# Performance work log

Measured on AMD Instinct MI355X. Metric: run time of the kernel, lower is better.

## Reference

```python
import jax, jax.numpy as jnp
import numpy as np

# SMPL/STAR kinematic tree: parent of joint i (i = 1..23)
PARENT = np.array([0, 0, 0, 1, 2, 3, 4, 5, 6, 7, 8, 9, 9, 9, 12, 13, 14, 16, 17, 18, 19, 20, 21])
B, V, J, NB = 512, 6890, 24, 10


def _axis_angle_parts(theta):
    # theta: [N,3] axis-angle. Matches STAR: norm of (theta + 1e-8).
    angle = jnp.linalg.norm(theta + 1e-8, axis=1, keepdims=True)  # [N,1]
    normalized = theta / angle
    half = angle * 0.5
    return jnp.cos(half), jnp.sin(half), normalized


def quat_feat(theta):
    c, s, n = _axis_angle_parts(theta)
    return jnp.concatenate([s * n, c - 1.0], axis=1)  # [N,4]


def rodrigues(theta):
    c, s, n = _axis_angle_parts(theta)
    w = c[:, 0]
    xyz = s * n
    x, y, z = xyz[:, 0], xyz[:, 1], xyz[:, 2]
    xx, yy, zz = x * x, y * y, z * z
    wx, wy, wz = w * x, w * y, w * z
    xy, xz, yz = x * y, x * z, y * z
    R = jnp.stack([
        1 - 2 * (yy + zz), 2 * (xy - wz), 2 * (xz + wy),
        2 * (xy + wz), 1 - 2 * (xx + zz), 2 * (yz - wx),
        2 * (xz - wy), 2 * (yz + wx), 1 - 2 * (xx + yy)], axis=-1)
    return R.reshape(-1, 3, 3)


def setup_inputs() -> dict:
    key = jax.random.key(0)
    ks = jax.random.split(key, 8)
    pose = jax.random.normal(ks[0], (B, 72), jnp.float32)
    betas = jax.random.normal(ks[1], (B, NB), jnp.float32)
    trans = jax.random.normal(ks[2], (B, 3), jnp.float32)
    v_template = jax.random.normal(ks[3], (V, 3), jnp.float32)
    shapedirs = jax.random.normal(ks[4], (V * 3, NB), jnp.float32) * 0.01
    posedirs = jax.random.normal(ks[5], (V * 3, 93), jnp.float32) * 0.01
    J_regressor = jax.random.uniform(ks[6], (J, V), jnp.float32)
    J_regressor = J_regressor / jnp.sum(J_regressor, axis=1, keepdims=True)
    weights = jax.random.uniform(ks[7], (V, J), jnp.float32)
    weights = weights / jnp.sum(weights, axis=1, keepdims=True)
    return {"pose": pose, "betas": betas, "trans": trans,
            "v_template": v_template, "shapedirs": shapedirs,
            "posedirs": posedirs, "J_regressor": J_regressor,
            "weights": weights}


def reference(pose, betas, trans, v_template, shapedirs, posedirs, J_regressor, weights):
    b = pose.shape[0]
    # shape blendshapes
    v_shaped = jnp.einsum('dk,bk->bd', shapedirs, betas).reshape(b, V, 3) + v_template[None]
    Jp = jnp.einsum('bik,ji->bjk', v_shaped, J_regressor)
    # pose features: quat feats of joints 1..23 + second beta
    pose_quat = quat_feat(pose.reshape(-1, 3)).reshape(b, -1)   # [b,96]
    pose_feat = jnp.concatenate([pose_quat[:, 4:], betas[:, 1:2]], axis=1)  # [b,93]
    R = rodrigues(pose.reshape(-1, 3)).reshape(b, J, 3, 3)
    # pose blendshapes
    v_posed = v_shaped + jnp.einsum('dk,bk->bd', posedirs, pose_feat).reshape(b, V, 3)
    # relative joint locations
    J_rel = jnp.concatenate([Jp[:, :1], Jp[:, 1:] - Jp[:, PARENT]], axis=1)  # [b,24,3]
    # local transforms [b,24,4,4]
    G_local = jnp.concatenate([R, J_rel[:, :, :, None]], axis=-1)
    pad = jnp.broadcast_to(jnp.array([0., 0., 0., 1.], jnp.float32).reshape(1, 1, 1, 4), (b, J, 1, 4))
    G_local = jnp.concatenate([G_local, pad], axis=2)
    # serial forward kinematics (fixed 24-joint chain)
    Gs = [G_local[:, 0]]
    for i in range(1, J):
        Gs.append(jnp.matmul(Gs[PARENT[i - 1]], G_local[:, i]))
    G = jnp.stack(Gs, axis=1)  # [b,24,4,4]
    posed_joints = G[:, :, :3, 3]
    # remove rest-pose joint transform: translation col -= R_part @ J
    t = jnp.einsum('bjxy,bjy->bjx', G[:, :, :3, :3], Jp)
    G_skin = G.at[:, :, :3, 3].add(-t)
    # skinning: T [b,6890,4,4]
    T = jnp.einsum('vj,bjxy->bvxy', weights, G_skin)
    v_h = jnp.concatenate([v_posed, jnp.ones((b, V, 1), v_posed.dtype)], axis=-1)
    v = jnp.einsum('bvxy,bvy->bvx', T, v_h)[:, :, :3] + trans[:, None, :]
    J_transformed = posed_joints + trans[:, None, :]
    return v, v_posed, v_shaped, J_transformed
```

## Files before the change

### kernel.cpp

```cpp
#include <hip/hip_runtime.h>

constexpr int kB  = 512;
constexpr int kV  = 6890;
constexpr int kJ  = 24;
constexpr int kD  = kV * 3;
constexpr int kNB = 10;
constexpr int kNF = 93;

__global__ __launch_bounds__(256) void kA_js(
    const float* __restrict__ Jreg, const float* __restrict__ shapedirs,
    const float* __restrict__ v_template, float* __restrict__ js,
    float* __restrict__ jt) {
  int jk = blockIdx.x;
  int j = jk / 3, k = jk % 3;
  int tid = threadIdx.x;
  float acc[kNB];
  float accT = 0.f;
#pragma unroll
  for (int nb = 0; nb < kNB; ++nb) acc[nb] = 0.f;
  for (int v = tid; v < kV; v += 256) {
    float w = Jreg[(size_t)j * kV + v];
    const float* srow = shapedirs + (size_t)(v * 3 + k) * kNB;
    accT += w * v_template[v * 3 + k];
#pragma unroll
    for (int nb = 0; nb < kNB; ++nb) acc[nb] += w * srow[nb];
  }
#pragma unroll
  for (int nb = 0; nb < kNB; ++nb)
#pragma unroll
    for (int off = 32; off > 0; off >>= 1)
      acc[nb] += __shfl_down(acc[nb], off, 64);
#pragma unroll
  for (int off = 32; off > 0; off >>= 1) accT += __shfl_down(accT, off, 64);
  __shared__ float red[4][11];
  int wave = tid >> 6, lane = tid & 63;
  if (lane == 0) {
#pragma unroll
    for (int nb = 0; nb < kNB; ++nb) red[wave][nb] = acc[nb];
    red[wave][10] = accT;
  }
  __syncthreads();
  if (tid == 0) {
#pragma unroll
    for (int nb = 0; nb < kNB; ++nb)
      js[jk * kNB + nb] = red[0][nb] + red[1][nb] + red[2][nb] + red[3][nb];
    jt[jk] = red[0][10] + red[1][10] + red[2][10] + red[3][10];
  }
}

__global__ __launch_bounds__(64) void kC_batch(
    const float* __restrict__ pose, const float* __restrict__ betas,
    const float* __restrict__ trans, const float* __restrict__ js,
    const float* __restrict__ jt, float* __restrict__ pfT,
    float* __restrict__ Gskin, float* __restrict__ out_Jt) {
  const int parent[24] = {-1, 0, 0, 0, 1, 2, 3, 4, 5, 6, 7, 8,
                          9, 9, 9, 12, 13, 14, 16, 17, 18, 19, 20, 21};
  const int depth[24] = {0, 1, 1, 1, 2, 2, 2, 3, 3, 3, 4, 4,
                         4, 4, 4, 5, 5, 5, 6, 6, 7, 7, 8, 8};
  int b = blockIdx.x;
  int j = threadIdx.x;
  __shared__ float G[24][12];
  __shared__ float Jp_s[24][3];
  float R[9];
  if (j < 24) {
    float t0 = pose[b * 72 + 3 * j + 0];
    float t1 = pose[b * 72 + 3 * j + 1];
    float t2 = pose[b * 72 + 3 * j + 2];
    float a0 = t0 + 1e-8f, a1 = t1 + 1e-8f, a2 = t2 + 1e-8f;
    float angle = sqrtf(a0 * a0 + a1 * a1 + a2 * a2);
    float inv = 1.0f / angle;
    float h = 0.5f * angle;
    float c = cosf(h), s = sinf(h);
    float x = s * t0 * inv, y = s * t1 * inv, z = s * t2 * inv, w = c;
    if (j >= 1) {
      int f = 4 * (j - 1);
      pfT[(size_t)(f + 0) * kB + b] = x;
      pfT[(size_t)(f + 1) * kB + b] = y;
      pfT[(size_t)(f + 2) * kB + b] = z;
      pfT[(size_t)(f + 3) * kB + b] = c - 1.0f;
    } else {
      pfT[(size_t)92 * kB + b] = betas[b * kNB + 1];
    }
    float xx = x * x, yy = y * y, zz = z * z;
    float wx = w * x, wy = w * y, wz = w * z;
    float xy = x * y, xz = x * z, yz = y * z;
    R[0] = 1.f - 2.f * (yy + zz); R[1] = 2.f * (xy - wz); R[2] = 2.f * (xz + wy);
    R[3] = 2.f * (xy + wz); R[4] = 1.f - 2.f * (xx + zz); R[5] = 2.f * (yz - wx);
    R[6] = 2.f * (xz - wy); R[7] = 2.f * (yz + wx); R[8] = 1.f - 2.f * (xx + yy);
    float bet[kNB];
#pragma unroll
    for (int nb = 0; nb < kNB; ++nb) bet[nb] = betas[b * kNB + nb];
#pragma unroll
    for (int k = 0; k < 3; ++k) {
      float a = jt[j * 3 + k];
      const float* jr = js + (size_t)(j * 3 + k) * kNB;
#pragma unroll
      for (int nb = 0; nb < kNB; ++nb) a += jr[nb] * bet[nb];
      Jp_s[j][k] = a;
    }
  }
  __syncthreads();
  float tl[3];
  if (j < 24) {
    int p = parent[j];
#pragma unroll
    for (int k = 0; k < 3; ++k)
      tl[k] = (p >= 0) ? (Jp_s[j][k] - Jp_s[p][k]) : Jp_s[j][k];
    if (j == 0) {
#pragma unroll
      for (int r = 0; r < 3; ++r) {
        G[0][r * 4 + 0] = R[r * 3 + 0];
        G[0][r * 4 + 1] = R[r * 3 + 1];
        G[0][r * 4 + 2] = R[r * 3 + 2];
        G[0][r * 4 + 3] = tl[r];
      }
    }
  }
  __syncthreads();
  for (int lev = 1; lev <= 8; ++lev) {
    if (j < 24 && depth[j] == lev) {
      int p = parent[j];
      float nG[12];
#pragma unroll
      for (int r = 0; r < 3; ++r) {
        float g0 = G[p][r * 4 + 0], g1 = G[p][r * 4 + 1];
        float g2 = G[p][r * 4 + 2], g3 = G[p][r * 4 + 3];
        nG[r * 4 + 0] = g0 * R[0] + g1 * R[3] + g2 * R[6];
        nG[r * 4 + 1] = g0 * R[1] + g1 * R[4] + g2 * R[7];
        nG[r * 4 + 2] = g0 * R[2] + g1 * R[5] + g2 * R[8];
        nG[r * 4 + 3] = g0 * tl[0] + g1 * tl[1] + g2 * tl[2] + g3;
      }
#pragma unroll
      for (int e = 0; e < 12; ++e) G[j][e] = nG[e];
    }
    __syncthreads();
  }
  if (j < 24) {
    float tr[3];
#pragma unroll
    for (int k = 0; k < 3; ++k) tr[k] = trans[b * 3 + k];
#pragma unroll
    for (int k = 0; k < 3; ++k)
      out_Jt[b * 72 + j * 3 + k] = G[j][k * 4 + 3] + tr[k];
    float jp0 = Jp_s[j][0], jp1 = Jp_s[j][1], jp2 = Jp_s[j][2];
    float* gs = Gskin + b * 288 + j * 12;
#pragma unroll
    for (int r = 0; r < 3; ++r) {
      float t = G[j][r * 4 + 0] * jp0 + G[j][r * 4 + 1] * jp1 + G[j][r * 4 + 2] * jp2;
      gs[r * 4 + 0] = G[j][r * 4 + 0];
      gs[r * 4 + 1] = G[j][r * 4 + 1];
      gs[r * 4 + 2] = G[j][r * 4 + 2];
      gs[r * 4 + 3] = G[j][r * 4 + 3] - t;
    }
  }
}

__global__ __launch_bounds__(256) void k14_fused(
    const float* __restrict__ shapedirs, const float* __restrict__ posedirs,
    const float* __restrict__ v_template, const float* __restrict__ betas,
    const float* __restrict__ pfT, float* __restrict__ out_vshaped,
    float* __restrict__ out_vposed) {
  int tid = threadIdx.x;
  int d = blockIdx.x * 256 + tid;
  bool active = d < kD;
  int dl = active ? d : (kD - 1);
  float sd[kNB], pd[kNF];
#pragma unroll
  for (int k = 0; k < kNB; ++k) sd[k] = shapedirs[(size_t)dl * kNB + k];
#pragma unroll
  for (int f = 0; f < kNF; ++f) pd[f] = posedirs[(size_t)dl * kNF + f];
  float vt = v_template[dl];
  int b0 = blockIdx.y * 32;
#pragma unroll 1
  for (int bc = 0; bc < 4; ++bc) {
    int bb = b0 + bc * 8;
    float as[8], ap[8];
#pragma unroll
    for (int t = 0; t < 8; ++t) {
      float a = vt;
#pragma unroll
      for (int k = 0; k < kNB; ++k) a += sd[k] * betas[(size_t)(bb + t) * kNB + k];
      as[t] = a;
      ap[t] = a;
    }
#pragma unroll
    for (int f = 0; f < kNF; ++f) {
      float pdf = pd[f];
      const float* q = pfT + (size_t)f * kB + bb;
#pragma unroll
      for (int t = 0; t < 8; ++t) ap[t] += pdf * q[t];
    }
    if (active) {
#pragma unroll
      for (int t = 0; t < 8; ++t) {
        size_t idx = (size_t)(bb + t) * kD + d;
        out_vshaped[idx] = as[t];
        out_vposed[idx] = ap[t];
      }
    }
  }
}

__global__ __launch_bounds__(256) void k5_skin(
    const float* __restrict__ weights, const float* __restrict__ Gskin,
    const float* __restrict__ trans, const float* __restrict__ vposed,
    float* __restrict__ out_v) {
  int tid = threadIdx.x;
  int v = blockIdx.x * 256 + tid;
  bool active = v < kV;
  int vl = active ? v : (kV - 1);
  float w[kJ];
#pragma unroll
  for (int j = 0; j < kJ; ++j) w[j] = weights[(size_t)vl * kJ + j];
  int b0 = blockIdx.y * 8;
#pragma unroll 1
  for (int bi = 0; bi < 8; ++bi) {
    int b = b0 + bi;
    const float* Gb = Gskin + (size_t)b * 288;
    float T[12];
#pragma unroll
    for (int e = 0; e < 12; ++e) T[e] = 0.f;
#pragma unroll
    for (int j = 0; j < kJ; ++j) {
      float wj = w[j];
#pragma unroll
      for (int e = 0; e < 12; ++e) T[e] += wj * Gb[j * 12 + e];
    }
    float tr0 = trans[b * 3 + 0];
    float tr1 = trans[b * 3 + 1];
    float tr2 = trans[b * 3 + 2];
    size_t base = (size_t)b * kD + (size_t)vl * 3;
    float q0 = vposed[base + 0];
    float q1 = vposed[base + 1];
    float q2 = vposed[base + 2];
    if (active) {
      out_v[base + 0] = T[0] * q0 + T[1] * q1 + T[2] * q2 + T[3] + tr0;
      out_v[base + 1] = T[4] * q0 + T[5] * q1 + T[6] * q2 + T[7] + tr1;
      out_v[base + 2] = T[8] * q0 + T[9] * q1 + T[10] * q2 + T[11] + tr2;
    }
  }
}

extern "C" void kernel_launch(void* const* d_in, const int* in_sizes, int n_in,
                              void* d_out, int out_size, void* d_ws,
                              size_t ws_size, hipStream_t stream) {
  const float* pose       = (const float*)d_in[0];
  const float* betas      = (const float*)d_in[1];
  const float* trans      = (const float*)d_in[2];
  const float* v_template = (const float*)d_in[3];
  const float* shapedirs  = (const float*)d_in[4];
  const float* posedirs   = (const float*)d_in[5];
  const float* Jreg       = (const float*)d_in[6];
  const float* weights    = (const float*)d_in[7];

  float* out = (float*)d_out;
  float* out_v       = out;
  float* out_vposed  = out + (size_t)kB * kD;
  float* out_vshaped = out + 2 * (size_t)kB * kD;
  float* out_Jt      = out + 3 * (size_t)kB * kD;

  float* wsf   = (float*)d_ws;
  float* pfT   = wsf;
  float* Gskin = pfT + kNF * kB;
  float* js    = Gskin + kB * 288;
  float* jt    = js + 72 * kNB;

  hipLaunchKernelGGL(kA_js, dim3(72), dim3(256), 0, stream, Jreg, shapedirs,
                     v_template, js, jt);
  hipLaunchKernelGGL(kC_batch, dim3(kB), dim3(64), 0, stream, pose, betas,
                     trans, js, jt, pfT, Gskin, out_Jt);
  hipLaunchKernelGGL(k14_fused, dim3((kD + 255) / 256, 16), dim3(256), 0,
                     stream, shapedirs, posedirs, v_template, betas, pfT,
                     out_vshaped, out_vposed);
  hipLaunchKernelGGL(k5_skin, dim3((kV + 255) / 256, 64), dim3(256), 0, stream,
                     weights, Gskin, trans, out_vposed, out_v);
}
```

Baseline: 267.1 us.

## Split joint-regressor reduction across blocks and widen batch tiles in blend and skin kernels

The joint-shape regression kernel now splits the vertex loop across 4 blocks per output and combines the partial sums with atomics, after a memset to zero the accumulators. The blend kernel processes 16 batch entries per inner chunk instead of 8 and writes v_shaped as soon as it is computed. The skinning kernel handles two batch entries per iteration for more instruction-level parallelism. The cost is extra register pressure, an added memset launch, and nondeterministic float summation order from the atomics.

```diff
diff --git a/kernel.cpp b/kernel.cpp
--- a/kernel.cpp
+++ b/kernel.cpp
@@ -18,7 +18,7 @@
   float accT = 0.f;
 #pragma unroll
   for (int nb = 0; nb < kNB; ++nb) acc[nb] = 0.f;
-  for (int v = tid; v < kV; v += 256) {
+  for (int v = blockIdx.y * 256 + tid; v < kV; v += 1024) {
     float w = Jreg[(size_t)j * kV + v];
     const float* srow = shapedirs + (size_t)(v * 3 + k) * kNB;
     accT += w * v_template[v * 3 + k];
@@ -43,8 +43,9 @@
   if (tid == 0) {
 #pragma unroll
     for (int nb = 0; nb < kNB; ++nb)
-      js[jk * kNB + nb] = red[0][nb] + red[1][nb] + red[2][nb] + red[3][nb];
-    jt[jk] = red[0][10] + red[1][10] + red[2][10] + red[3][10];
+      atomicAdd(&js[jk * kNB + nb],
+                red[0][nb] + red[1][nb] + red[2][nb] + red[3][nb]);
+    atomicAdd(&jt[jk], red[0][10] + red[1][10] + red[2][10] + red[3][10]);
   }
 }
 
@@ -172,31 +173,29 @@
   float vt = v_template[dl];
   int b0 = blockIdx.y * 32;
 #pragma unroll 1
-  for (int bc = 0; bc < 4; ++bc) {
-    int bb = b0 + bc * 8;
-    float as[8], ap[8];
-#pragma unroll
-    for (int t = 0; t < 8; ++t) {
+  for (int bc = 0; bc < 2; ++bc) {
+    int bb = b0 + bc * 16;
+    float ap[16];
+#pragma unroll
+    for (int t = 0; t < 16; ++t) {
+      const float* be = betas + (size_t)(bb + t) * kNB;
       float a = vt;
 #pragma unroll
-      for (int k = 0; k < kNB; ++k) a += sd[k] * betas[(size_t)(bb + t) * kNB + k];
-      as[t] = a;
+      for (int k = 0; k < kNB; ++k) a += sd[k] * be[k];
       ap[t] = a;
+      if (active) out_vshaped[(size_t)(bb + t) * kD + d] = a;
     }
 #pragma unroll
     for (int f = 0; f < kNF; ++f) {
       float pdf = pd[f];
       const float* q = pfT + (size_t)f * kB + bb;
 #pragma unroll
-      for (int t = 0; t < 8; ++t) ap[t] += pdf * q[t];
+      for (int t = 0; t < 16; ++t) ap[t] += pdf * q[t];
     }
     if (active) {
 #pragma unroll
-      for (int t = 0; t < 8; ++t) {
-        size_t idx = (size_t)(bb + t) * kD + d;
-        out_vshaped[idx] = as[t];
-        out_vposed[idx] = ap[t];
-      }
+      for (int t = 0; t < 16; ++t)
+        out_vposed[(size_t)(bb + t) * kD + d] = ap[t];
     }
   }
 }
@@ -214,29 +213,36 @@
   for (int j = 0; j < kJ; ++j) w[j] = weights[(size_t)vl * kJ + j];
   int b0 = blockIdx.y * 8;
 #pragma unroll 1
-  for (int bi = 0; bi < 8; ++bi) {
-    int b = b0 + bi;
-    const float* Gb = Gskin + (size_t)b * 288;
-    float T[12];
-#pragma unroll
-    for (int e = 0; e < 12; ++e) T[e] = 0.f;
+  for (int bp = 0; bp < 4; ++bp) {
+    int bA = b0 + bp * 2;
+    int bBt = bA + 1;
+    const float* GA = Gskin + (size_t)bA * 288;
+    const float* GB = Gskin + (size_t)bBt * 288;
+    float TA[12], TB[12];
+#pragma unroll
+    for (int e = 0; e < 12; ++e) { TA[e] = 0.f; TB[e] = 0.f; }
 #pragma unroll
     for (int j = 0; j < kJ; ++j) {
       float wj = w[j];
 #pragma unroll
-      for (int e = 0; e < 12; ++e) T[e] += wj * Gb[j * 12 + e];
-    }
-    float tr0 = trans[b * 3 + 0];
-    float tr1 = trans[b * 3 + 1];
-    float tr2 = trans[b * 3 + 2];
-    size_t base = (size_t)b * kD + (size_t)vl * 3;
-    float q0 = vposed[base + 0];
-    float q1 = vposed[base + 1];
-    float q2 = vposed[base + 2];
+      for (int e = 0; e < 12; ++e) {
+        TA[e] += wj * GA[j * 12 + e];
+        TB[e] += wj * GB[j * 12 + e];
+      }
+    }
+    float trA0 = trans[bA * 3 + 0], trA1 = trans[bA * 3 + 1], trA2 = trans[bA * 3 + 2];
+    float trB0 = trans[bBt * 3 + 0], trB1 = trans[bBt * 3 + 1], trB2 = trans[bBt * 3 + 2];
+    size_t baseA = (size_t)bA * kD + (size_t)vl * 3;
+    size_t baseB = (size_t)bBt * kD + (size_t)vl * 3;
+    float a0 = vposed[baseA + 0], a1 = vposed[baseA + 1], a2 = vposed[baseA + 2];
+    float b0v = vposed[baseB + 0], b1v = vposed[baseB + 1], b2v = vposed[baseB + 2];
     if (active) {
-      out_v[base + 0] = T[0] * q0 + T[1] * q1 + T[2] * q2 + T[3] + tr0;
-      out_v[base + 1] = T[4] * q0 + T[5] * q1 + T[6] * q2 + T[7] + tr1;
-      out_v[base + 2] = T[8] * q0 + T[9] * q1 + T[10] * q2 + T[11] + tr2;
+      out_v[baseA + 0] = TA[0] * a0 + TA[1] * a1 + TA[2] * a2 + TA[3] + trA0;
+      out_v[baseA + 1] = TA[4] * a0 + TA[5] * a1 + TA[6] * a2 + TA[7] + trA1;
+      out_v[baseA + 2] = TA[8] * a0 + TA[9] * a1 + TA[10] * a2 + TA[11] + trA2;
+      out_v[baseB + 0] = TB[0] * b0v + TB[1] * b1v + TB[2] * b2v + TB[3] + trB0;
+      out_v[baseB + 1] = TB[4] * b0v + TB[5] * b1v + TB[6] * b2v + TB[7] + trB1;
+      out_v[baseB + 2] = TB[8] * b0v + TB[9] * b1v + TB[10] * b2v + TB[11] + trB2;
     }
   }
 }
@@ -265,7 +271,9 @@
   float* js    = Gskin + kB * 288;
   float* jt    = js + 72 * kNB;
 
-  hipLaunchKernelGGL(kA_js, dim3(72), dim3(256), 0, stream, Jreg, shapedirs,
+  hipMemsetAsync(js, 0, (72 * kNB + 72) * sizeof(float), stream);
+
+  hipLaunchKernelGGL(kA_js, dim3(72, 4), dim3(256), 0, stream, Jreg, shapedirs,
                      v_template, js, jt);
   hipLaunchKernelGGL(kC_batch, dim3(kB), dim3(64), 0, stream, pose, betas,
                      trans, js, jt, pfT, Gskin, out_Jt);
```

Result: slower. 287.1 us (+7.5%).

## Split joint-shape reduction across blocks and stage skin transforms in LDS

Applied to the files above, without the earlier changes.

The joint-regressor reduction kernel now runs 4x more blocks, each covering a strided quarter of the vertices, and combines partial sums with atomicAdd into buffers zeroed by a memset. The skinning kernel cooperatively loads the 8 batches' joint transforms into shared memory and reads them as float4, replacing repeated global scalar loads. A small pointer hoist for betas is also added. The extra memset launch and atomics add overhead, and float atomic summation order is nondeterministic.

```diff
diff --git a/kernel.cpp b/kernel.cpp
--- a/kernel.cpp
+++ b/kernel.cpp
@@ -18,7 +18,7 @@
   float accT = 0.f;
 #pragma unroll
   for (int nb = 0; nb < kNB; ++nb) acc[nb] = 0.f;
-  for (int v = tid; v < kV; v += 256) {
+  for (int v = blockIdx.y * 256 + tid; v < kV; v += 1024) {
     float w = Jreg[(size_t)j * kV + v];
     const float* srow = shapedirs + (size_t)(v * 3 + k) * kNB;
     accT += w * v_template[v * 3 + k];
@@ -43,8 +43,9 @@
   if (tid == 0) {
 #pragma unroll
     for (int nb = 0; nb < kNB; ++nb)
-      js[jk * kNB + nb] = red[0][nb] + red[1][nb] + red[2][nb] + red[3][nb];
-    jt[jk] = red[0][10] + red[1][10] + red[2][10] + red[3][10];
+      atomicAdd(&js[jk * kNB + nb],
+                red[0][nb] + red[1][nb] + red[2][nb] + red[3][nb]);
+    atomicAdd(&jt[jk], red[0][10] + red[1][10] + red[2][10] + red[3][10]);
   }
 }
 
@@ -177,9 +178,10 @@
     float as[8], ap[8];
 #pragma unroll
     for (int t = 0; t < 8; ++t) {
+      const float* be = betas + (size_t)(bb + t) * kNB;
       float a = vt;
 #pragma unroll
-      for (int k = 0; k < kNB; ++k) a += sd[k] * betas[(size_t)(bb + t) * kNB + k];
+      for (int k = 0; k < kNB; ++k) a += sd[k] * be[k];
       as[t] = a;
       ap[t] = a;
     }
@@ -205,6 +207,7 @@
     const float* __restrict__ weights, const float* __restrict__ Gskin,
     const float* __restrict__ trans, const float* __restrict__ vposed,
     float* __restrict__ out_v) {
+  __shared__ __align__(16) float Gs[8 * 288];
   int tid = threadIdx.x;
   int v = blockIdx.x * 256 + tid;
   bool active = v < kV;
@@ -213,30 +216,40 @@
 #pragma unroll
   for (int j = 0; j < kJ; ++j) w[j] = weights[(size_t)vl * kJ + j];
   int b0 = blockIdx.y * 8;
+  {
+    const float* src = Gskin + (size_t)b0 * 288;
+#pragma unroll
+    for (int i = 0; i < 9; ++i) Gs[i * 256 + tid] = src[i * 256 + tid];
+  }
+  __syncthreads();
 #pragma unroll 1
   for (int bi = 0; bi < 8; ++bi) {
     int b = b0 + bi;
-    const float* Gb = Gskin + (size_t)b * 288;
-    float T[12];
-#pragma unroll
-    for (int e = 0; e < 12; ++e) T[e] = 0.f;
-#pragma unroll
-    for (int j = 0; j < kJ; ++j) {
-      float wj = w[j];
-#pragma unroll
-      for (int e = 0; e < 12; ++e) T[e] += wj * Gb[j * 12 + e];
-    }
-    float tr0 = trans[b * 3 + 0];
-    float tr1 = trans[b * 3 + 1];
-    float tr2 = trans[b * 3 + 2];
     size_t base = (size_t)b * kD + (size_t)vl * 3;
     float q0 = vposed[base + 0];
     float q1 = vposed[base + 1];
     float q2 = vposed[base + 2];
+    float tr0 = trans[b * 3 + 0];
+    float tr1 = trans[b * 3 + 1];
+    float tr2 = trans[b * 3 + 2];
+    const float4* Gt = (const float4*)(Gs + bi * 288);
+    float T0 = 0.f, T1 = 0.f, T2 = 0.f, T3 = 0.f;
+    float T4 = 0.f, T5 = 0.f, T6 = 0.f, T7 = 0.f;
+    float T8 = 0.f, T9 = 0.f, T10 = 0.f, T11 = 0.f;
+#pragma unroll 4
+    for (int j = 0; j < kJ; ++j) {
+      float wj = w[j];
+      float4 ga = Gt[j * 3 + 0];
+      float4 gb = Gt[j * 3 + 1];
+      float4 gc = Gt[j * 3 + 2];
+      T0 += wj * ga.x; T1 += wj * ga.y; T2 += wj * ga.z; T3 += wj * ga.w;
+      T4 += wj * gb.x; T5 += wj * gb.y; T6 += wj * gb.z; T7 += wj * gb.w;
+      T8 += wj * gc.x; T9 += wj * gc.y; T10 += wj * gc.z; T11 += wj * gc.w;
+    }
     if (active) {
-      out_v[base + 0] = T[0] * q0 + T[1] * q1 + T[2] * q2 + T[3] + tr0;
-      out_v[base + 1] = T[4] * q0 + T[5] * q1 + T[6] * q2 + T[7] + tr1;
-      out_v[base + 2] = T[8] * q0 + T[9] * q1 + T[10] * q2 + T[11] + tr2;
+      out_v[base + 0] = T0 * q0 + T1 * q1 + T2 * q2 + T3 + tr0;
+      out_v[base + 1] = T4 * q0 + T5 * q1 + T6 * q2 + T7 + tr1;
+      out_v[base + 2] = T8 * q0 + T9 * q1 + T10 * q2 + T11 + tr2;
     }
   }
 }
@@ -265,7 +278,9 @@
   float* js    = Gskin + kB * 288;
   float* jt    = js + 72 * kNB;
 
-  hipLaunchKernelGGL(kA_js, dim3(72), dim3(256), 0, stream, Jreg, shapedirs,
+  hipMemsetAsync(js, 0, (72 * kNB + 72) * sizeof(float), stream);
+
+  hipLaunchKernelGGL(kA_js, dim3(72, 4), dim3(256), 0, stream, Jreg, shapedirs,
                      v_template, js, jt);
   hipLaunchKernelGGL(kC_batch, dim3(kB), dim3(64), 0, stream, pose, betas,
                      trans, js, jt, pfT, Gskin, out_Jt);
```

Measured after the change: 252.2 us. 5.6% less time.
